# Kernel tuning notes

Measured on AMD Instinct MI355X. Metric: run time of the kernel, lower is better.

Reference implementation:

```python
import jax, jax.numpy as jnp
import numpy as np
from jax import lax

B, N, D = 8, 16384, 64
NPOINT, NSAMPLE, RADIUS = 1024, 32, 0.1
MLP = [3 + D, 64, 64, 128]
BN_EPS = 1e-5


def setup_inputs() -> dict:
    key = jax.random.key(0)
    ks = jax.random.split(key, 8)
    inp = {
        'xyz': jax.random.uniform(ks[0], (B, 3, N), dtype=jnp.float32),
        'points': jax.random.normal(ks[1], (B, D, N), dtype=jnp.float32),
    }
    for i, (cin, cout) in enumerate(zip(MLP[:-1], MLP[1:]), start=1):
        inp[f'w{i}'] = jax.random.normal(ks[1 + i], (cout, cin), dtype=jnp.float32) / np.sqrt(cin)
        inp[f'b{i}'] = jnp.zeros((cout,), jnp.float32)
        inp[f'g{i}'] = jnp.ones((cout,), jnp.float32)
        inp[f'be{i}'] = jnp.zeros((cout,), jnp.float32)
    return inp


def farthest_point_sample(xyz, npoint):
    # xyz: (B, N, 3). Deterministic start at index 0 (torch uses randint).
    b, n, _ = xyz.shape

    def step(carry, _):
        distance, farthest = carry  # (B,N), (B,)
        centroid = jnp.take_along_axis(xyz, farthest[:, None, None], axis=1)  # (B,1,3)
        dist = jnp.sum((xyz - centroid) ** 2, axis=-1)  # (B,N)
        distance = jnp.minimum(distance, dist)
        new_far = jnp.argmax(distance, axis=-1).astype(jnp.int32)
        return (distance, new_far), farthest

    init = (jnp.full((b, n), 1e10, xyz.dtype), jnp.zeros((b,), jnp.int32))
    _, idxs = lax.scan(step, init, None, length=npoint)  # (npoint, B)
    return idxs.T  # (B, npoint)


def query_ball_point(radius, nsample, xyz, new_xyz):
    # xyz: (B,N,3), new_xyz: (B,S,3) -> (B,S,nsample) int32
    b, n, _ = xyz.shape
    # squared pairwise distances (B,S,N)
    sqr = (jnp.sum(new_xyz ** 2, -1)[:, :, None]
           + jnp.sum(xyz ** 2, -1)[:, None, :]
           - 2.0 * jnp.einsum('bsc,bnc->bsn', new_xyz, xyz))
    group_idx = jnp.where(sqr > radius ** 2, n, jnp.arange(n, dtype=jnp.int32))
    group_idx = jnp.sort(group_idx, axis=-1)[:, :, :nsample]
    first = group_idx[:, :, :1]
    return jnp.where(group_idx == n, first, group_idx)


def reference(xyz, points, w1, b1, g1, be1, w2, b2, g2, be2, w3, b3, g3, be3):
    xyz_t = xyz.transpose(0, 2, 1)      # (B,N,3)
    pts_t = points.transpose(0, 2, 1)   # (B,N,D)
    bsz = xyz_t.shape[0]

    fps_idx = farthest_point_sample(xyz_t, NPOINT)          # (B,S)
    bidx2 = jnp.arange(bsz)[:, None]
    new_xyz = xyz_t[bidx2, fps_idx]                          # (B,S,3)

    idx = query_ball_point(RADIUS, NSAMPLE, xyz_t, new_xyz)  # (B,S,ns)
    bidx3 = jnp.arange(bsz)[:, None, None]
    grouped_xyz = xyz_t[bidx3, idx] - new_xyz[:, :, None, :]  # (B,S,ns,3)
    grouped_pts = pts_t[bidx3, idx]                           # (B,S,ns,D)
    feat = jnp.concatenate([grouped_xyz, grouped_pts], axis=-1)  # (B,S,ns,C)

    for w, b, g, be in ((w1, b1, g1, be1), (w2, b2, g2, be2), (w3, b3, g3, be3)):
        feat = jnp.einsum('bsnc,oc->bsno', feat, w) + b
        mean = feat.mean(axis=(0, 1, 2))
        var = feat.var(axis=(0, 1, 2))  # biased, as torch BN uses for normalization
        feat = (feat - mean) * lax.rsqrt(var + BN_EPS) * g + be
        feat = jax.nn.relu(feat)

    new_points = feat.max(axis=2)  # max over nsample -> (B,S,Cout)
    return new_xyz.transpose(0, 2, 1), new_points.transpose(0, 2, 1)
```

## Files before the change

### kernel.cpp

```cpp
#include <hip/hip_runtime.h>
#include <hip/hip_bf16.h>
#include <stdint.h>

#define BATCH 8
#define NPTS  16384
#define DIMF  64
#define SPTS  1024
#define NSAMP 32
#define MTOT  (BATCH*SPTS*NSAMP)

__device__ __forceinline__ float bfu_lo(uint32_t u){ return __uint_as_float(u<<16); }
__device__ __forceinline__ float bfu_hi(uint32_t u){ return __uint_as_float(u & 0xffff0000u); }
__device__ __forceinline__ uint16_t f2bf(float f){
  __hip_bfloat16 h = __float2bfloat16(f);
  uint16_t u; __builtin_memcpy(&u, &h, 2); return u;
}

__global__ __launch_bounds__(256) void transpose_kernel(const float* __restrict__ pts,
                                                        float* __restrict__ ptsT){
  __shared__ float tile[32][33];
  int b = blockIdx.z;
  int n0 = blockIdx.x*32, c0 = blockIdx.y*32;
  int tx = threadIdx.x & 31, ty = threadIdx.x >> 5;
  const float* src = pts + (size_t)b*DIMF*NPTS;
  float* dst = ptsT + (size_t)b*NPTS*DIMF;
#pragma unroll
  for (int j=0;j<4;j++)
    tile[ty+8*j][tx] = src[(size_t)(c0+ty+8*j)*NPTS + n0 + tx];
  __syncthreads();
#pragma unroll
  for (int j=0;j<4;j++)
    dst[(size_t)(n0+ty+8*j)*DIMF + c0 + tx] = tile[tx][ty+8*j];
}

__global__ __launch_bounds__(512, 2) void fps_kernel(const float* __restrict__ xyz,
                                                     float* __restrict__ out0){
  int b = blockIdx.x;
  const float* X = xyz + (size_t)b*3*NPTS;
  int t = threadIdx.x;
  int lane = t & 63, wid = t >> 6;
  float px[32], py[32], pz[32], dst[32];
#pragma unroll
  for (int k=0;k<32;k++){
    int n = t + (k<<9);
    px[k]=X[n]; py[k]=X[NPTS+n]; pz[k]=X[2*NPTS+n];
    dst[k]=1e10f;
  }
#pragma unroll
  for (int k=0;k<32;k++){
    asm volatile("" : "+v"(px[k]), "+v"(py[k]), "+v"(pz[k]));
  }
  __shared__ float rv[2][8];
  __shared__ int   ri[2][8];
  int far = 0;
  float* o = out0 + (size_t)b*3*SPTS;
  for (int s=0;s<SPTS;s++){
    float cx = X[far], cy = X[NPTS+far], cz = X[2*NPTS+far];
    if (t==0){ o[s]=cx; o[SPTS+s]=cy; o[2*SPTS+s]=cz; }
    if (s==SPTS-1) break;
    float best = -1.0f; int bi = 0x7fffffff;
#pragma unroll
    for (int k=0;k<32;k++){
      float dx=__fsub_rn(px[k],cx), dy=__fsub_rn(py[k],cy), dz=__fsub_rn(pz[k],cz);
      float d = __fadd_rn(__fadd_rn(__fmul_rn(dx,dx),__fmul_rn(dy,dy)),__fmul_rn(dz,dz));
      d = fminf(dst[k], d); dst[k] = d;
      if (d > best){ best = d; bi = t + (k<<9); }
    }
#pragma unroll
    for (int off=1; off<64; off<<=1){
      float ov = __shfl_xor(best, off);
      int   oi = __shfl_xor(bi, off);
      if (ov > best || (ov == best && oi < bi)){ best = ov; bi = oi; }
    }
    int p = s & 1;
    if (lane==0){ rv[p][wid]=best; ri[p][wid]=bi; }
    __syncthreads();
    float v = rv[p][lane&7]; int j = ri[p][lane&7];
#pragma unroll
    for (int off=1; off<8; off<<=1){
      float ov = __shfl_xor(v, off);
      int   oj = __shfl_xor(j, off);
      if (ov > v || (ov == v && oj < j)){ v = ov; j = oj; }
    }
    far = __builtin_amdgcn_readfirstlane(j);
  }
}

__global__ __launch_bounds__(256) void ball_kernel(const float* __restrict__ xyz,
                                                   const float* __restrict__ newxyz,
                                                   int* __restrict__ idxo){
  int b  = blockIdx.x >> 5;
  int sc = blockIdx.x & 31;
  const float* X  = xyz + (size_t)b*3*NPTS;
  int t = threadIdx.x, lane = t & 63, w = t >> 6;
  __shared__ float lx[512], ly[512], lz[512], ls[512];
  __shared__ int done;
  if (t==0) done = 0;
  const float rsq = 0.01f;
  float nx[8], ny[8], nz[8], sn[8];
  int cnt[8], first[8];
  int sbase = sc*32 + w*8;
#pragma unroll
  for (int q=0;q<8;q++){
    int s = sbase + q;
    nx[q] = newxyz[(size_t)b*3*SPTS + s];
    ny[q] = newxyz[(size_t)b*3*SPTS + SPTS + s];
    nz[q] = newxyz[(size_t)b*3*SPTS + 2*SPTS + s];
    sn[q] = __fadd_rn(__fadd_rn(__fmul_rn(nx[q],nx[q]),__fmul_rn(ny[q],ny[q])),
                      __fmul_rn(nz[q],nz[q]));
    cnt[q]=0; first[q]=0;
  }
  __syncthreads();
  for (int T=0;T<32;T++){
    {
      float ax = X[T*512 + t], ay = X[NPTS + T*512 + t], az = X[2*NPTS + T*512 + t];
      lx[t]=ax; ly[t]=ay; lz[t]=az;
      ls[t] = __fadd_rn(__fadd_rn(__fmul_rn(ax,ax),__fmul_rn(ay,ay)),__fmul_rn(az,az));
      float bx = X[T*512 + t + 256], by = X[NPTS + T*512 + t + 256], bz = X[2*NPTS + T*512 + t + 256];
      lx[t+256]=bx; ly[t+256]=by; lz[t+256]=bz;
      ls[t+256] = __fadd_rn(__fadd_rn(__fmul_rn(bx,bx),__fmul_rn(by,by)),__fmul_rn(bz,bz));
    }
    __syncthreads();
#pragma unroll
    for (int q=0;q<8;q++){
      if (cnt[q] >= NSAMP) continue;
      int s = sbase + q;
      int* op = idxo + ((size_t)(b*SPTS + s))*NSAMP;
      for (int c=0;c<8;c++){
        int li = c*64 + lane;
        float dot = fmaf(nz[q], lz[li], fmaf(ny[q], ly[li], __fmul_rn(nx[q], lx[li])));
        float sq  = __fsub_rn(__fadd_rn(sn[q], ls[li]), __fmul_rn(2.0f, dot));
        bool in = (sq <= rsq);
        unsigned long long m = __ballot(in);
        if (cnt[q]==0 && m) first[q] = T*512 + c*64 + (int)__builtin_ctzll(m);
        if (in){
          int slot = cnt[q] + (int)__popcll(m & ((1ull<<lane)-1ull));
          if (slot < NSAMP) op[slot] = T*512 + li;
        }
        cnt[q] += (int)__popcll(m);
        if (cnt[q] >= NSAMP){ if (lane==0) atomicAdd(&done,1); break; }
      }
    }
    __syncthreads();
    if (done >= 32) break;
  }
#pragma unroll
  for (int q=0;q<8;q++){
    if (cnt[q] < NSAMP){
      int s = sbase + q;
      int* op = idxo + ((size_t)(b*SPTS + s))*NSAMP;
      if (lane >= cnt[q] && lane < NSAMP) op[lane] = first[q];
    }
  }
}

__global__ __launch_bounds__(256) void gemm1_kernel(const float* __restrict__ xyz,
                                                    const float* __restrict__ ptsT,
                                                    const int* __restrict__ idx,
                                                    const float* __restrict__ newxyz,
                                                    const float* __restrict__ w1,
                                                    const float* __restrict__ b1,
                                                    uint16_t* __restrict__ y1){
  __shared__ float As[128*69];
  __shared__ float Ws[67*64];
  __shared__ float bias[64];
  __shared__ int   ndx[128];
  __shared__ float nxs[4][3];
  int t = threadIdx.x;
  int g0 = blockIdx.x*128;
  if (t < 128) ndx[t] = idx[g0 + t];
  if (t < 12){
    int grp = t/3, c = t%3;
    int bs = (g0>>5) + grp; int b = bs>>10, s = bs & 1023;
    nxs[grp][c] = newxyz[(size_t)b*3*SPTS + c*SPTS + s];
  }
  if (t < 64) bias[t] = b1[t];
  for (int e=t; e<67*64; e+=256){ int k=e>>6, c=e&63; Ws[k*64+c] = w1[c*67+k]; }
  __syncthreads();
  {
    int r = t>>1, h = t&1;
    int n = ndx[r];
    int bs = (g0>>5) + (r>>5); int b = bs>>10;
    const float* pr = ptsT + ((size_t)(b*NPTS + n))*64 + h*32;
    float* ar = As + r*69;
    if (h==0){
      int grp = r>>5;
      ar[0] = __fsub_rn(xyz[(size_t)b*3*NPTS + n],          nxs[grp][0]);
      ar[1] = __fsub_rn(xyz[(size_t)b*3*NPTS + NPTS + n],   nxs[grp][1]);
      ar[2] = __fsub_rn(xyz[(size_t)b*3*NPTS + 2*NPTS + n], nxs[grp][2]);
    }
    float* ap = ar + 3 + h*32;
#pragma unroll
    for (int j=0;j<8;j++){
      float4 v = *(const float4*)(pr + j*4);
      ap[j*4+0]=v.x; ap[j*4+1]=v.y; ap[j*4+2]=v.z; ap[j*4+3]=v.w;
    }
  }
  __syncthreads();
  int rg = t>>3, cg = t&7;
  float acc[4][8];
#pragma unroll
  for (int i=0;i<4;i++)
#pragma unroll
    for (int j=0;j<8;j++) acc[i][j]=0.f;
  for (int k=0;k<67;k++){
    float a0 = As[(rg*4+0)*69+k];
    float a1 = As[(rg*4+1)*69+k];
    float a2 = As[(rg*4+2)*69+k];
    float a3 = As[(rg*4+3)*69+k];
    const float* wr = Ws + k*64 + cg*8;
    float4 w0 = *(const float4*)wr;
    float4 w1v = *(const float4*)(wr+4);
    float wj[8] = {w0.x,w0.y,w0.z,w0.w,w1v.x,w1v.y,w1v.z,w1v.w};
#pragma unroll
    for (int j=0;j<8;j++){
      acc[0][j] = fmaf(a0, wj[j], acc[0][j]);
      acc[1][j] = fmaf(a1, wj[j], acc[1][j]);
      acc[2][j] = fmaf(a2, wj[j], acc[2][j]);
      acc[3][j] = fmaf(a3, wj[j], acc[3][j]);
    }
  }
#pragma unroll
  for (int i=0;i<4;i++){
    int gr = g0 + rg*4 + i;
    uint16_t* yr = y1 + (size_t)gr*64 + cg*8;
    uint4 vv;
    uint32_t u[4];
#pragma unroll
    for (int j=0;j<4;j++){
      float v0 = acc[i][2*j]   + bias[cg*8+2*j];
      float v1 = acc[i][2*j+1] + bias[cg*8+2*j+1];
      u[j] = (uint32_t)f2bf(v0) | ((uint32_t)f2bf(v1)<<16);
    }
    vv.x=u[0]; vv.y=u[1]; vv.z=u[2]; vv.w=u[3];
    *(uint4*)yr = vv;
  }
}

__global__ __launch_bounds__(256) void gemm2_kernel(const uint16_t* __restrict__ yin,
                                                    const float* __restrict__ w2,
                                                    const float* __restrict__ b2,
                                                    const float* __restrict__ scale,
                                                    const float* __restrict__ shift,
                                                    uint16_t* __restrict__ yout){
  __shared__ float As[128*65];
  __shared__ float Ws[64*64];
  __shared__ float bias[64], sc[64], sh[64];
  int t = threadIdx.x;
  int g0 = blockIdx.x*128;
  if (t < 64){ bias[t]=b2[t]; sc[t]=scale[t]; sh[t]=shift[t]; }
  for (int e=t; e<64*64; e+=256){ int k=e>>6, c=e&63; Ws[k*64+c] = w2[c*64+k]; }
  __syncthreads();
  {
    int r = t>>1, h = t&1;
    const uint4* yv = (const uint4*)(yin + (size_t)(g0+r)*64 + h*32);
    float* ar = As + r*65 + h*32;
#pragma unroll
    for (int j=0;j<4;j++){
      uint4 u = yv[j];
      uint32_t vv[4] = {u.x,u.y,u.z,u.w};
#pragma unroll
      for (int m=0;m<4;m++){
        int c = h*32 + j*8 + m*2;
        ar[j*8+m*2]   = fmaxf(fmaf(bfu_lo(vv[m]), sc[c],   sh[c]),   0.f);
        ar[j*8+m*2+1] = fmaxf(fmaf(bfu_hi(vv[m]), sc[c+1], sh[c+1]), 0.f);
      }
    }
  }
  __syncthreads();
  int rg = t>>3, cg = t&7;
  float acc[4][8];
#pragma unroll
  for (int i=0;i<4;i++)
#pragma unroll
    for (int j=0;j<8;j++) acc[i][j]=0.f;
  for (int k=0;k<64;k++){
    float a0 = As[(rg*4+0)*65+k];
    float a1 = As[(rg*4+1)*65+k];
    float a2 = As[(rg*4+2)*65+k];
    float a3 = As[(rg*4+3)*65+k];
    const float* wr = Ws + k*64 + cg*8;
    float4 w0 = *(const float4*)wr;
    float4 w1v = *(const float4*)(wr+4);
    float wj[8] = {w0.x,w0.y,w0.z,w0.w,w1v.x,w1v.y,w1v.z,w1v.w};
#pragma unroll
    for (int j=0;j<8;j++){
      acc[0][j] = fmaf(a0, wj[j], acc[0][j]);
      acc[1][j] = fmaf(a1, wj[j], acc[1][j]);
      acc[2][j] = fmaf(a2, wj[j], acc[2][j]);
      acc[3][j] = fmaf(a3, wj[j], acc[3][j]);
    }
  }
#pragma unroll
  for (int i=0;i<4;i++){
    int gr = g0 + rg*4 + i;
    uint16_t* yr = yout + (size_t)gr*64 + cg*8;
    uint4 vv; uint32_t u[4];
#pragma unroll
    for (int j=0;j<4;j++){
      float v0 = acc[i][2*j]   + bias[cg*8+2*j];
      float v1 = acc[i][2*j+1] + bias[cg*8+2*j+1];
      u[j] = (uint32_t)f2bf(v0) | ((uint32_t)f2bf(v1)<<16);
    }
    vv.x=u[0]; vv.y=u[1]; vv.z=u[2]; vv.w=u[3];
    *(uint4*)yr = vv;
  }
}

__global__ __launch_bounds__(256) void gemm3_kernel(const uint16_t* __restrict__ yin,
                                                    const float* __restrict__ w3,
                                                    const float* __restrict__ b3,
                                                    const float* __restrict__ scale,
                                                    const float* __restrict__ shift,
                                                    uint16_t* __restrict__ yout){
  __shared__ float As[64*65];
  __shared__ float Ws[64*128];
  __shared__ float bias[128], sc[64], sh[64];
  int t = threadIdx.x;
  int g0 = blockIdx.x*64;
  if (t < 128) bias[t]=b3[t];
  if (t < 64){ sc[t]=scale[t]; sh[t]=shift[t]; }
  for (int e=t; e<64*128; e+=256){ int k=e>>7, c=e&127; Ws[k*128+c] = w3[c*64+k]; }
  __syncthreads();
  {
    int r = t>>2, h = t&3;
    const uint4* yv = (const uint4*)(yin + (size_t)(g0+r)*64 + h*16);
    float* ar = As + r*65 + h*16;
#pragma unroll
    for (int j=0;j<2;j++){
      uint4 u = yv[j];
      uint32_t vv[4] = {u.x,u.y,u.z,u.w};
#pragma unroll
      for (int m=0;m<4;m++){
        int c = h*16 + j*8 + m*2;
        ar[j*8+m*2]   = fmaxf(fmaf(bfu_lo(vv[m]), sc[c],   sh[c]),   0.f);
        ar[j*8+m*2+1] = fmaxf(fmaf(bfu_hi(vv[m]), sc[c+1], sh[c+1]), 0.f);
      }
    }
  }
  __syncthreads();
  int rg = t>>4, cg = t&15;
  float acc[4][8];
#pragma unroll
  for (int i=0;i<4;i++)
#pragma unroll
    for (int j=0;j<8;j++) acc[i][j]=0.f;
  for (int k=0;k<64;k++){
    float a0 = As[(rg*4+0)*65+k];
    float a1 = As[(rg*4+1)*65+k];
    float a2 = As[(rg*4+2)*65+k];
    float a3 = As[(rg*4+3)*65+k];
    const float* wr = Ws + k*128 + cg*8;
    float4 w0 = *(const float4*)wr;
    float4 w1v = *(const float4*)(wr+4);
    float wj[8] = {w0.x,w0.y,w0.z,w0.w,w1v.x,w1v.y,w1v.z,w1v.w};
#pragma unroll
    for (int j=0;j<8;j++){
      acc[0][j] = fmaf(a0, wj[j], acc[0][j]);
      acc[1][j] = fmaf(a1, wj[j], acc[1][j]);
      acc[2][j] = fmaf(a2, wj[j], acc[2][j]);
      acc[3][j] = fmaf(a3, wj[j], acc[3][j]);
    }
  }
#pragma unroll
  for (int i=0;i<4;i++){
    int gr = g0 + rg*4 + i;
    uint16_t* yr = yout + (size_t)gr*128 + cg*8;
    uint4 vv; uint32_t u[4];
#pragma unroll
    for (int j=0;j<4;j++){
      float v0 = acc[i][2*j]   + bias[cg*8+2*j];
      float v1 = acc[i][2*j+1] + bias[cg*8+2*j+1];
      u[j] = (uint32_t)f2bf(v0) | ((uint32_t)f2bf(v1)<<16);
    }
    vv.x=u[0]; vv.y=u[1]; vv.z=u[2]; vv.w=u[3];
    *(uint4*)yr = vv;
  }
}

template<int C>
__global__ __launch_bounds__(256) void stats_kernel(const uint16_t* __restrict__ y,
                                                    float* __restrict__ gsum,
                                                    float* __restrict__ gsq){
  constexpr int CP  = C/2;
  constexpr int RSL = 256/CP;
  int t = threadIdx.x;
  int c0 = t % CP, rs = t / CP;
  float s0=0.f,q0=0.f,s1=0.f,q1=0.f;
#pragma unroll 4
  for (int i=0;i<512/RSL;i++){
    int r = blockIdx.x*512 + rs + i*RSL;
    uint32_t u = *(const uint32_t*)(y + (size_t)r*C + 2*c0);
    float v0 = bfu_lo(u), v1 = bfu_hi(u);
    s0 += v0; q0 += v0*v0; s1 += v1; q1 += v1*v1;
  }
  __shared__ float red[4][256];
  red[0][t]=s0; red[1][t]=q0; red[2][t]=s1; red[3][t]=q1;
  __syncthreads();
  if (t < CP){
    float a0=0,a1=0,a2=0,a3=0;
    for (int k=0;k<RSL;k++){
      a0+=red[0][k*CP+t]; a1+=red[1][k*CP+t]; a2+=red[2][k*CP+t]; a3+=red[3][k*CP+t];
    }
    atomicAdd(&gsum[2*t],   a0); atomicAdd(&gsq[2*t],   a1);
    atomicAdd(&gsum[2*t+1], a2); atomicAdd(&gsq[2*t+1], a3);
  }
}

__global__ void finalize_kernel(const float* __restrict__ gsum, const float* __restrict__ gsq,
                                const float* __restrict__ g, const float* __restrict__ be,
                                float* __restrict__ scale, float* __restrict__ shift, int C){
  int c = threadIdx.x;
  if (c >= C) return;
  double mean = (double)gsum[c] / (double)MTOT;
  double var  = (double)gsq[c] / (double)MTOT - mean*mean;
  double s    = (double)g[c] / sqrt(var + 1e-5);
  scale[c] = (float)s;
  shift[c] = (float)((double)be[c] - mean*s);
}

__global__ __launch_bounds__(256) void maxpool_kernel(const uint16_t* __restrict__ y3,
                                                      const float* __restrict__ scale,
                                                      const float* __restrict__ shift,
                                                      float* __restrict__ out1){
  __shared__ float tr[16][129];
  int t = threadIdx.x;
  int b = blockIdx.x >> 6;
  int s0 = (blockIdx.x & 63) * 16;
  int ch = t & 127, sl0 = t >> 7;
  float scv = scale[ch], shv = shift[ch];
  for (int sl=sl0; sl<16; sl+=2){
    int bs = b*SPTS + s0 + sl;
    const uint16_t* yr = y3 + (size_t)bs*NSAMP*128 + ch;
    float m = 0.0f;
#pragma unroll 4
    for (int k=0;k<NSAMP;k++){
      float v = __uint_as_float(((uint32_t)yr[k*128])<<16);
      float z = fmaxf(fmaf(v, scv, shv), 0.f);
      m = fmaxf(m, z);
    }
    tr[sl][ch] = m;
  }
  __syncthreads();
  int ch2 = t >> 1, hh = t & 1;
  float vals[8];
#pragma unroll
  for (int i=0;i<8;i++) vals[i] = tr[hh*8+i][ch2];
  float* op = out1 + (size_t)b*131072 + (size_t)ch2*1024 + s0 + hh*8;
  float4 v0; v0.x=vals[0]; v0.y=vals[1]; v0.z=vals[2]; v0.w=vals[3];
  float4 v1; v1.x=vals[4]; v1.y=vals[5]; v1.z=vals[6]; v1.w=vals[7];
  *(float4*)op = v0;
  *(float4*)(op+4) = v1;
}

extern "C" void kernel_launch(void* const* d_in, const int* in_sizes, int n_in,
                              void* d_out, int out_size, void* d_ws, size_t ws_size,
                              hipStream_t stream){
  (void)in_sizes; (void)n_in; (void)out_size; (void)ws_size;
  const float* xyz = (const float*)d_in[0];
  const float* pts = (const float*)d_in[1];
  const float* w1 = (const float*)d_in[2];  const float* b1 = (const float*)d_in[3];
  const float* g1 = (const float*)d_in[4];  const float* be1 = (const float*)d_in[5];
  const float* w2 = (const float*)d_in[6];  const float* b2 = (const float*)d_in[7];
  const float* g2 = (const float*)d_in[8];  const float* be2 = (const float*)d_in[9];
  const float* w3 = (const float*)d_in[10]; const float* b3 = (const float*)d_in[11];
  const float* g3 = (const float*)d_in[12]; const float* be3 = (const float*)d_in[13];

  float* out0 = (float*)d_out;
  float* out1 = out0 + BATCH*3*SPTS;

  char* ws = (char*)d_ws;
  float*    ptsT = (float*)(ws + 0);
  int*      idx  = (int*)  (ws + 34078720);
  uint16_t* y1   = (uint16_t*)(ws + 35127296);
  uint16_t* y2   = (uint16_t*)(ws + 68681728);
  uint16_t* y3   = (uint16_t*)(ws + 102236160);
  float*    stats = (float*)(ws + 169345024);
  float* gsum1 = stats;        float* gsq1 = stats + 128;
  float* gsum2 = stats + 256;  float* gsq2 = stats + 384;
  float* gsum3 = stats + 512;  float* gsq3 = stats + 640;
  float* scale1 = stats + 768; float* shift1 = stats + 896;
  float* scale2 = stats + 1024; float* shift2 = stats + 1152;
  float* scale3 = stats + 1280; float* shift3 = stats + 1408;

  hipMemsetAsync(stats, 0, 768*sizeof(float), stream);

  transpose_kernel<<<dim3(NPTS/32, DIMF/32, BATCH), 256, 0, stream>>>(pts, ptsT);
  fps_kernel<<<BATCH, 512, 0, stream>>>(xyz, out0);
  ball_kernel<<<BATCH*32, 256, 0, stream>>>(xyz, out0, idx);
  gemm1_kernel<<<MTOT/128, 256, 0, stream>>>(xyz, ptsT, idx, out0, w1, b1, y1);
  stats_kernel<64><<<512, 256, 0, stream>>>(y1, gsum1, gsq1);
  finalize_kernel<<<1, 128, 0, stream>>>(gsum1, gsq1, g1, be1, scale1, shift1, 64);
  gemm2_kernel<<<MTOT/128, 256, 0, stream>>>(y1, w2, b2, scale1, shift1, y2);
  stats_kernel<64><<<512, 256, 0, stream>>>(y2, gsum2, gsq2);
  finalize_kernel<<<1, 128, 0, stream>>>(gsum2, gsq2, g2, be2, scale2, shift2, 64);
  gemm3_kernel<<<MTOT/64, 256, 0, stream>>>(y2, w3, b3, scale2, shift2, y3);
  stats_kernel<128><<<512, 256, 0, stream>>>(y3, gsum3, gsq3);
  finalize_kernel<<<1, 128, 0, stream>>>(gsum3, gsq3, g3, be3, scale3, shift3, 128);
  maxpool_kernel<<<BATCH*(SPTS/16), 256, 0, stream>>>(y3, scale3, shift3, out1);
}
```

Measured before the change: 2.633 ms.

## Accelerate farthest point sampling with spatial grid cells and lower-bound pruning

The FPS kernel now bins points into an 8x8x8 grid, stores them sorted by cell in a workspace buffer, and keeps per-cell maximum distances in shared memory. Each iteration only rescans cells whose box lower bound to the new centroid could lower their current max, instead of updating all 16384 points. This is meant to cut the serial per-iteration cost of FPS, which dominates the pipeline with only 8 blocks. In exchange it adds a setup sort, divergent per-cell work that depends on the data, and 64-bit packed argmax reductions. It also reuses part of the y1 workspace region, which is safe only because gemm1 runs after FPS.

Measured after the change: 3.225 ms. +22.5%, slower.

```diff
diff --git a/kernel.cpp b/kernel.cpp
--- a/kernel.cpp
+++ b/kernel.cpp
@@ -8,12 +8,19 @@
 #define SPTS  1024
 #define NSAMP 32
 #define MTOT  (BATCH*SPTS*NSAMP)
+#define CELLS 512
 
 __device__ __forceinline__ float bfu_lo(uint32_t u){ return __uint_as_float(u<<16); }
 __device__ __forceinline__ float bfu_hi(uint32_t u){ return __uint_as_float(u & 0xffff0000u); }
 __device__ __forceinline__ uint16_t f2bf(float f){
   __hip_bfloat16 h = __float2bfloat16(f);
   uint16_t u; __builtin_memcpy(&u, &h, 2); return u;
+}
+
+__device__ __forceinline__ unsigned long long shfl_xor_u64(unsigned long long v, int off){
+  unsigned lo = (unsigned)v, hi = (unsigned)(v>>32);
+  lo = __shfl_xor(lo, off); hi = __shfl_xor(hi, off);
+  return ((unsigned long long)hi<<32) | lo;
 }
 
 __global__ __launch_bounds__(256) void transpose_kernel(const float* __restrict__ pts,
@@ -33,56 +40,154 @@
     dst[(size_t)(n0+ty+8*j)*DIMF + c0 + tx] = tile[tx][ty+8*j];
 }
 
-__global__ __launch_bounds__(512, 2) void fps_kernel(const float* __restrict__ xyz,
-                                                     float* __restrict__ out0){
+__device__ __forceinline__ int cell_of(float x, float y, float z){
+  int ix=(int)(x*8.0f); ix = ix<0?0:(ix>7?7:ix);
+  int iy=(int)(y*8.0f); iy = iy<0?0:(iy>7?7:iy);
+  int iz=(int)(z*8.0f); iz = iz<0?0:(iz>7?7:iz);
+  return (ix<<6)|(iy<<3)|iz;
+}
+
+__global__ __launch_bounds__(512) void fps_kernel(const float* __restrict__ xyz,
+                                                  float* __restrict__ out0,
+                                                  float4* __restrict__ sortg){
   int b = blockIdx.x;
   const float* X = xyz + (size_t)b*3*NPTS;
-  int t = threadIdx.x;
-  int lane = t & 63, wid = t >> 6;
-  float px[32], py[32], pz[32], dst[32];
+  float4* sp = sortg + (size_t)b*NPTS;
+  int t = threadIdx.x, lane = t & 63, w = t >> 6;
+
+  __shared__ float dst_s[NPTS];
+  __shared__ int   hist[CELLS];
+  __shared__ int   cursor[CELLS];
+  __shared__ int   cstart[CELLS+1];
+  __shared__ float cmaxv[CELLS];
+  __shared__ int   cmaxk[CELLS];
+  __shared__ float cwx[CELLS], cwy[CELLS], cwz[CELLS];
+  __shared__ int   wsum[8];
+  __shared__ float4 pf4[2][8];
+  __shared__ unsigned long long pk64[2][8];
+
+  if (t < CELLS) hist[t] = 0;
+  __syncthreads();
 #pragma unroll
   for (int k=0;k<32;k++){
     int n = t + (k<<9);
-    px[k]=X[n]; py[k]=X[NPTS+n]; pz[k]=X[2*NPTS+n];
-    dst[k]=1e10f;
-  }
+    atomicAdd(&hist[cell_of(X[n],X[NPTS+n],X[2*NPTS+n])],1);
+  }
+  __syncthreads();
+  {
+    int v = hist[t], inc = v;
+#pragma unroll
+    for (int off=1; off<64; off<<=1){ int u=__shfl_up(inc,off); if(lane>=off) inc+=u; }
+    if (lane==63) wsum[w] = inc;
+    __syncthreads();
+    if (t==0){ int acc=0; for(int i=0;i<8;i++){int x=wsum[i]; wsum[i]=acc; acc+=x;} }
+    __syncthreads();
+    int ex = inc - v + wsum[w];
+    cstart[t]=ex; cursor[t]=ex;
+    cmaxv[t] = (v>0)?1e10f:0.0f;
+    cmaxk[t] = 16383;
+    if (t==0) cstart[CELLS]=NPTS;
+  }
+  __syncthreads();
 #pragma unroll
   for (int k=0;k<32;k++){
-    asm volatile("" : "+v"(px[k]), "+v"(py[k]), "+v"(pz[k]));
-  }
-  __shared__ float rv[2][8];
-  __shared__ int   ri[2][8];
-  int far = 0;
+    int n = t + (k<<9);
+    float x=X[n], y=X[NPTS+n], z=X[2*NPTS+n];
+    int c = cell_of(x,y,z);
+    int pos = atomicAdd(&cursor[c],1);
+    sp[pos] = make_float4(x,y,z,__int_as_float(n));
+  }
+  for (int n=t;n<NPTS;n+=512) dst_s[n]=1e10f;
+  __syncthreads();
+
+  int ix = (((lane>>5)&1)<<2) | (((lane>>4)&1)<<1) | ((w>>2)&1);
+  int iy = (((lane>>3)&1)<<2) | (((lane>>2)&1)<<1) | ((w>>1)&1);
+  int iz = (((lane>>1)&1)<<2) | (( lane    &1)<<1) | ( w    &1);
+  int cm = (ix<<6)|(iy<<3)|iz;
+  float lox=ix*0.125f, loy=iy*0.125f, loz=iz*0.125f;
+
+  float cx=X[0], cy=X[NPTS], cz=X[2*NPTS];
   float* o = out0 + (size_t)b*3*SPTS;
   for (int s=0;s<SPTS;s++){
-    float cx = X[far], cy = X[NPTS+far], cz = X[2*NPTS+far];
     if (t==0){ o[s]=cx; o[SPTS+s]=cy; o[2*SPTS+s]=cz; }
     if (s==SPTS-1) break;
-    float best = -1.0f; int bi = 0x7fffffff;
-#pragma unroll
-    for (int k=0;k<32;k++){
-      float dx=__fsub_rn(px[k],cx), dy=__fsub_rn(py[k],cy), dz=__fsub_rn(pz[k],cz);
-      float d = __fadd_rn(__fadd_rn(__fmul_rn(dx,dx),__fmul_rn(dy,dy)),__fmul_rn(dz,dz));
-      d = fminf(dst[k], d); dst[k] = d;
-      if (d > best){ best = d; bi = t + (k<<9); }
-    }
-#pragma unroll
-    for (int off=1; off<64; off<<=1){
-      float ov = __shfl_xor(best, off);
-      int   oi = __shfl_xor(bi, off);
-      if (ov > best || (ov == best && oi < bi)){ best = ov; bi = oi; }
-    }
+    float dxx = fmaxf(fmaxf(lox-cx, cx-(lox+0.125f)),0.f);
+    float dyy = fmaxf(fmaxf(loy-cy, cy-(loy+0.125f)),0.f);
+    float dzz = fmaxf(fmaxf(loz-cz, cz-(loz+0.125f)),0.f);
+    float lb = dxx*dxx+dyy*dyy+dzz*dzz;
+    bool dirty = (lb*(1.0f-4e-6f)-4e-6f) < cmaxv[cm];
+    unsigned long long mask = __ballot(dirty);
+    while (mask){
+      int l = (int)__builtin_ctzll(mask); mask &= mask-1;
+      int jx = (((l>>5)&1)<<2) | (((l>>4)&1)<<1) | ((w>>2)&1);
+      int jy = (((l>>3)&1)<<2) | (((l>>2)&1)<<1) | ((w>>1)&1);
+      int jz = (((l>>1)&1)<<2) | (( l    &1)<<1) | ( w    &1);
+      int c = (jx<<6)|(jy<<3)|jz;
+      int st = cstart[c], en = cstart[c+1];
+      if (st >= en) continue;
+      unsigned long long bp = 0ull; float bd=0.f,bx=0.f,by=0.f,bz=0.f;
+      for (int base=st; base<en; base+=64){
+        int pos = base+lane;
+        if (pos<en){
+          float4 pq = sp[pos];
+          float ddx=__fsub_rn(pq.x,cx), ddy=__fsub_rn(pq.y,cy), ddz=__fsub_rn(pq.z,cz);
+          float d = __fadd_rn(__fadd_rn(__fmul_rn(ddx,ddx),__fmul_rn(ddy,ddy)),
+                              __fmul_rn(ddz,ddz));
+          float od = dst_s[pos];
+          d = fminf(od, d);
+          dst_s[pos] = d;
+          int orig = __float_as_int(pq.w);
+          unsigned long long pk =
+            ((unsigned long long)__float_as_uint(d)<<32) | (unsigned)(16383-orig);
+          if (pk > bp){ bp=pk; bd=d; bx=pq.x; by=pq.y; bz=pq.z; }
+        }
+      }
+      unsigned long long rp = bp;
+#pragma unroll
+      for (int off=1; off<64; off<<=1){
+        unsigned long long op = shfl_xor_u64(rp, off);
+        rp = (op>rp)? op : rp;
+      }
+      unsigned long long wm = __ballot(bp==rp);
+      int wl = (int)__builtin_ctzll(wm);
+      if (lane==wl){
+        cmaxv[c]=bd;
+        cmaxk[c]=16383-(int)(bp & 0xffffffffull);
+        cwx[c]=bx; cwy[c]=by; cwz[c]=bz;
+      }
+    }
+    __builtin_amdgcn_wave_barrier();
     int p = s & 1;
-    if (lane==0){ rv[p][wid]=best; ri[p][wid]=bi; }
+    {
+      float v = cmaxv[cm]; int kk = cmaxk[cm];
+      unsigned long long p2 =
+        ((unsigned long long)__float_as_uint(v)<<32) | (unsigned)(16383-kk);
+      unsigned long long r2 = p2;
+#pragma unroll
+      for (int off=1; off<64; off<<=1){
+        unsigned long long o2 = shfl_xor_u64(r2, off);
+        r2 = (o2>r2)? o2 : r2;
+      }
+      unsigned long long wm2 = __ballot(p2==r2);
+      int wl2 = (int)__builtin_ctzll(wm2);
+      if (lane==wl2){
+        pf4[p][w] = make_float4(cwx[cm], cwy[cm], cwz[cm], 0.f);
+        pk64[p][w] = r2;
+      }
+    }
     __syncthreads();
-    float v = rv[p][lane&7]; int j = ri[p][lane&7];
-#pragma unroll
-    for (int off=1; off<8; off<<=1){
-      float ov = __shfl_xor(v, off);
-      int   oj = __shfl_xor(j, off);
-      if (ov > v || (ov == v && oj < j)){ v = ov; j = oj; }
-    }
-    far = __builtin_amdgcn_readfirstlane(j);
+    {
+      unsigned long long fv = pk64[p][lane&7], fr = fv;
+#pragma unroll
+      for (int off=1; off<8; off<<=1){
+        unsigned long long of = shfl_xor_u64(fr, off);
+        fr = (of>fr)? of : fr;
+      }
+      unsigned long long fm = __ballot(fv==fr);
+      int fl = (int)__builtin_ctzll(fm) & 7;
+      float4 cc = pf4[p][fl];
+      cx=cc.x; cy=cc.y; cz=cc.z;
+    }
   }
 }
 
@@ -476,6 +581,7 @@
   uint16_t* y2   = (uint16_t*)(ws + 68681728);
   uint16_t* y3   = (uint16_t*)(ws + 102236160);
   float*    stats = (float*)(ws + 169345024);
+  float4* sortg = (float4*)(ws + 35127296);
   float* gsum1 = stats;        float* gsq1 = stats + 128;
   float* gsum2 = stats + 256;  float* gsq2 = stats + 384;
   float* gsum3 = stats + 512;  float* gsq3 = stats + 640;
@@ -486,7 +592,7 @@
   hipMemsetAsync(stats, 0, 768*sizeof(float), stream);
 
   transpose_kernel<<<dim3(NPTS/32, DIMF/32, BATCH), 256, 0, stream>>>(pts, ptsT);
-  fps_kernel<<<BATCH, 512, 0, stream>>>(xyz, out0);
+  fps_kernel<<<BATCH, 512, 0, stream>>>(xyz, out0, sortg);
   ball_kernel<<<BATCH*32, 256, 0, stream>>>(xyz, out0, idx);
   gemm1_kernel<<<MTOT/128, 256, 0, stream>>>(xyz, ptsT, idx, out0, w1, b1, y1);
   stats_kernel<64><<<512, 256, 0, stream>>>(y1, gsum1, gsq1);
```
